# Kernel tuning notes

Measured on AMD Instinct MI355X. Metric: run time of the kernel, lower is better.

Reference implementation:

```python
import jax, jax.numpy as jnp
import numpy as np

NEG_SLOPE = 0.2  # PyG GATConv default negative_slope
N_NODES = 10000
N_EDGES = 320000
IN_CH = 512
HID = 128
HEADS = 4
N_CLASSES = 2


def gat_conv(x, src, dst, n, W, att_src, att_dst, bias, concat):
    """PyG-style GATConv (shared weights for src/dst, eval mode: no dropout)."""
    H, C = att_src.shape
    h = (x @ W).reshape(-1, H, C)                      # [N, H, C]
    a_src = jnp.sum(h * att_src[None], axis=-1)        # [N, H]
    a_dst = jnp.sum(h * att_dst[None], axis=-1)        # [N, H]
    e = a_src[src] + a_dst[dst]                        # [E, H]
    e = jnp.where(e > 0, e, NEG_SLOPE * e)             # LeakyReLU
    # numerically stable softmax over incoming edges of each dst node
    m = jax.ops.segment_max(e, dst, num_segments=n)    # [N, H]
    m = jnp.where(jnp.isfinite(m), m, 0.0)
    ex = jnp.exp(e - m[dst])
    denom = jax.ops.segment_sum(ex, dst, num_segments=n)
    alpha = ex / (denom[dst] + 1e-16)                  # [E, H]
    out = jax.ops.segment_sum(alpha[:, :, None] * h[src], dst, num_segments=n)  # [N,H,C]
    if concat:
        out = out.reshape(n, H * C)
    else:
        out = out.mean(axis=1)
    return out + bias


def setup_inputs() -> dict:
    key = jax.random.key(0)
    ks = jax.random.split(key, 8)
    x = jax.random.normal(ks[0], (N_NODES, IN_CH), dtype=jnp.float32)
    edge_index = jax.random.randint(ks[1], (2, N_EDGES), 0, N_NODES, dtype=jnp.int32)
    s1 = 1.0 / np.sqrt(IN_CH)
    s2 = 1.0 / np.sqrt(HEADS * HID)
    return {
        "x": x,
        "edge_index": edge_index,
        "W1": jax.random.normal(ks[2], (IN_CH, HEADS * HID), dtype=jnp.float32) * s1,
        "att_src1": jax.random.normal(ks[3], (HEADS, HID), dtype=jnp.float32) * s2,
        "att_dst1": jax.random.normal(ks[4], (HEADS, HID), dtype=jnp.float32) * s2,
        "b1": jnp.zeros((HEADS * HID,), dtype=jnp.float32),
        "W2": jax.random.normal(ks[5], (HEADS * HID, N_CLASSES), dtype=jnp.float32) * s2,
        "att_src2": jax.random.normal(ks[6], (1, N_CLASSES), dtype=jnp.float32),
        "att_dst2": jax.random.normal(ks[7], (1, N_CLASSES), dtype=jnp.float32),
        "b2": jnp.zeros((N_CLASSES,), dtype=jnp.float32),
    }


def reference(x, edge_index, W1, att_src1, att_dst1, b1, W2, att_src2, att_dst2, b2):
    n = x.shape[0]
    loop = jnp.arange(n, dtype=edge_index.dtype)       # PyG add_self_loops=True
    src = jnp.concatenate([edge_index[0], loop])
    dst = jnp.concatenate([edge_index[1], loop])
    h = gat_conv(x, src, dst, n, W1, att_src1, att_dst1, b1, concat=True)
    h = jax.nn.elu(h)
    out = gat_conv(h, src, dst, n, W2, att_src2, att_dst2, b2, concat=False)
    return out
```

## Files before the change

kernel.cpp:

```cpp
#include <hip/hip_runtime.h>
#include <hip/hip_bf16.h>

#define N_NODES 10000
#define N_EDGES 320000
#define E_TOT   330000
#define IN_CH   512
#define F1      512
#define HID     128
#define HEADS   4
#define SLOTS   128
#define MAXDEG  64

typedef __attribute__((ext_vector_type(8))) short bf16x8;
typedef __attribute__((ext_vector_type(4))) float f32x4;

__device__ __forceinline__ float lo16(unsigned u) { return __uint_as_float(u << 16); }
__device__ __forceinline__ float hi16(unsigned u) { return __uint_as_float(u & 0xffff0000u); }
__device__ __forceinline__ unsigned short bfbits(float f) {
    __hip_bfloat16 h = __float2bfloat16(f);
    return *(unsigned short*)&h;
}

__device__ __forceinline__ void gload_lds16(const void* g, void* l) {
    __builtin_amdgcn_global_load_lds(
        (const __attribute__((address_space(1))) unsigned int*)g,
        (__attribute__((address_space(3))) unsigned int*)l, 16, 0, 0);
}

__global__ void k_prep(const float* __restrict__ x, unsigned short* __restrict__ xb,
                       const float* __restrict__ w1, unsigned short* __restrict__ w1t,
                       int* __restrict__ zbase) {
    __shared__ float tile[64][65];
    int b = blockIdx.x;
    int t = threadIdx.x;
    if (b < 5000) {
        int idx = b * 256 + t;
        float4 v = ((const float4*)x)[idx];
        ushort4 u;
        u.x = bfbits(v.x); u.y = bfbits(v.y); u.z = bfbits(v.z); u.w = bfbits(v.w);
        ((ushort4*)xb)[idx] = u;
    } else if (b < 5064) {
        int bb = b - 5000;
        int bi = bb >> 3, bj = bb & 7;
        int r0 = t >> 6, col = t & 63;
#pragma unroll
        for (int p = 0; p < 16; ++p) {
            int row = p * 4 + r0;
            tile[row][col] = w1[(size_t)(bi * 64 + row) * 512 + bj * 64 + col];
        }
        __syncthreads();
#pragma unroll
        for (int p = 0; p < 16; ++p) {
            int row = p * 4 + r0;
            w1t[(size_t)(bj * 64 + row) * 512 + bi * 64 + col] = bfbits(tile[col][row]);
        }
    } else {
        int idx = (b - 5064) * 256 + t;
        if (idx < 130000) zbase[idx] = 0;
    }
}

#define GEMM_BLKS 316
__device__ __forceinline__ void gemm_step(const __hip_bfloat16* A, const __hip_bfloat16* B,
                                          int wr, int wc, int col16, int quad,
                                          f32x4 acc[4][4]) {
#pragma unroll
    for (int kk = 0; kk < 2; ++kk) {
        bf16x8 af[4], bf[4];
#pragma unroll
        for (int m = 0; m < 4; ++m) {
            int r = wr * 64 + m * 16 + col16;
            af[m] = *(const bf16x8*)((const char*)A + r * 128 +
                                     ((kk * 64 + quad * 16) ^ ((r & 7) << 4)));
        }
#pragma unroll
        for (int c = 0; c < 4; ++c) {
            int r = wc * 64 + c * 16 + col16;
            bf[c] = *(const bf16x8*)((const char*)B + r * 128 +
                                     ((kk * 64 + quad * 16) ^ ((r & 7) << 4)));
        }
#pragma unroll
        for (int m = 0; m < 4; ++m)
#pragma unroll
            for (int c = 0; c < 4; ++c)
                acc[m][c] = __builtin_amdgcn_mfma_f32_16x16x32_bf16(af[m], bf[c], acc[m][c], 0, 0, 0);
    }
}

__global__ __launch_bounds__(256) void k_gemm1(const __hip_bfloat16* __restrict__ xb,
                                               const __hip_bfloat16* __restrict__ w1t,
                                               const float* __restrict__ as_vec,
                                               const float* __restrict__ ad_vec,
                                               __hip_bfloat16* __restrict__ h1b,
                                               float* __restrict__ a_src,
                                               float* __restrict__ a_dst,
                                               const int* __restrict__ src,
                                               const int* __restrict__ dst,
                                               int* __restrict__ cnt,
                                               int* __restrict__ slots) {
    if (blockIdx.x >= GEMM_BLKS) {
        int e = (blockIdx.x - GEMM_BLKS) * 256 + threadIdx.x;
        if (e < E_TOT) {
            int d, s;
            if (e < N_EDGES) { d = dst[e]; s = src[e]; } else { d = e - N_EDGES; s = d; }
            int pos = atomicAdd(&cnt[d], 1);
            if (pos < SLOTS) slots[d * SLOTS + pos] = s;
        }
        return;
    }
    __shared__ __align__(16) __hip_bfloat16 lsA[2][128 * 64];
    __shared__ __align__(16) __hip_bfloat16 lsB[2][128 * 64];
    int nt = blockIdx.x & 3;
    int mt = blockIdx.x >> 2;
    int row0 = mt * 128;
    int t = threadIdx.x;
    int lane = t & 63;
    int wid = t >> 6;
    int wr = wid >> 1, wc = wid & 1;
    int col16 = lane & 15, quad = lane >> 4;

    const __hip_bfloat16* ga[4];
    const __hip_bfloat16* gb[4];
    unsigned loff[4];
#pragma unroll
    for (int p = 0; p < 4; ++p) {
        int ci = p * 256 + t;
        int row = ci >> 3, ch = ci & 7;
        int sch = ch ^ (row & 7);
        ga[p] = xb + (size_t)min(row0 + row, N_NODES - 1) * IN_CH + sch * 8;
        gb[p] = w1t + (size_t)(nt * 128 + row) * IN_CH + sch * 8;
        loff[p] = ci * 16;
    }

    f32x4 acc[4][4] = {};

#pragma unroll
    for (int p = 0; p < 4; ++p) gload_lds16(ga[p], (char*)lsA[0] + loff[p]);
#pragma unroll
    for (int p = 0; p < 4; ++p) gload_lds16(gb[p], (char*)lsB[0] + loff[p]);
    __syncthreads();

#pragma unroll 1
    for (int s = 0; s < 7; ++s) {
        int nb = (s + 1) & 1, kt = (s + 1) * 64;
#pragma unroll
        for (int p = 0; p < 4; ++p) gload_lds16(ga[p] + kt, (char*)lsA[nb] + loff[p]);
#pragma unroll
        for (int p = 0; p < 4; ++p) gload_lds16(gb[p] + kt, (char*)lsB[nb] + loff[p]);
        gemm_step(lsA[s & 1], lsB[s & 1], wr, wc, col16, quad, acc);
        __syncthreads();
    }
    gemm_step(lsA[1], lsB[1], wr, wc, col16, quad, acc);

    float asv[4], adv[4];
#pragma unroll
    for (int c = 0; c < 4; ++c) {
        int col = nt * 128 + wc * 64 + c * 16 + col16;
        asv[c] = as_vec[col];
        adv[c] = ad_vec[col];
    }
#pragma unroll
    for (int m = 0; m < 4; ++m) {
#pragma unroll
        for (int reg = 0; reg < 4; ++reg) {
            int row = row0 + wr * 64 + m * 16 + quad * 4 + reg;
            bool ok = row < N_NODES;
            float ps = 0.f, pd = 0.f;
#pragma unroll
            for (int c = 0; c < 4; ++c) {
                float v = acc[m][c][reg];
                ps += v * asv[c];
                pd += v * adv[c];
                if (ok) h1b[(size_t)row * F1 + nt * 128 + wc * 64 + c * 16 + col16] =
                            __float2bfloat16(v);
            }
#pragma unroll
            for (int off = 1; off <= 8; off <<= 1) {
                ps += __shfl_xor(ps, off);
                pd += __shfl_xor(pd, off);
            }
            if (col16 == 0 && ok) {
                atomicAdd(&a_src[row * HEADS + nt], ps);
                atomicAdd(&a_dst[row * HEADS + nt], pd);
            }
        }
    }
}

__global__ __launch_bounds__(256, 8) void k_aggr1(const __hip_bfloat16* __restrict__ h1b,
                                               const float* __restrict__ a_src,
                                               const float* __restrict__ a_dst,
                                               const int* __restrict__ cnt,
                                               const int* __restrict__ slots,
                                               const float* __restrict__ b1,
                                               const float* __restrict__ w2,
                                               const float* __restrict__ as2,
                                               const float* __restrict__ ad2,
                                               float* __restrict__ h2,
                                               float* __restrict__ a_src2,
                                               float* __restrict__ a_dst2) {
    __shared__ int2 wlds[4][MAXDEG];
    int h = blockIdx.x & 3;
    int wslot = threadIdx.x >> 6;
    int n = (blockIdx.x >> 2) * 4 + wslot;
    int lane = threadIdx.x & 63;
    int cn = min(cnt[n], MAXDEG);
    const int* sl = slots + n * SLOTS;
    float adst = a_dst[n * HEADS + h];

    int jc = min(lane, cn - 1);
    int s = sl[jc];
    float e = a_src[s * HEADS + h] + adst;
    e = fmaxf(e, 0.2f * e);
    float w = (lane < cn) ? __expf(e) : 0.f;
    float dsum = w;
#pragma unroll
    for (int off = 1; off < 64; off <<= 1) dsum += __shfl_xor(dsum, off);
    int2 pw; pw.x = s << 10;
    pw.y = __float_as_int(w);
    wlds[wslot][lane] = pw;
    __syncthreads();

    int q = lane >> 4, c16 = lane & 15;
    const char* hb = (const char*)h1b + (h * 128 + c16 * 8) * 2;
    float acc[8] = {};
#pragma unroll 1
    for (int base = 0; base < cn; base += 16) {
        int2 p[4];
#pragma unroll
        for (int k = 0; k < 4; ++k) p[k] = wlds[wslot][base + k * 4 + q];
        uint4 d[4];
#pragma unroll
        for (int k = 0; k < 4; ++k) d[k] = *(const uint4*)(hb + p[k].x);
#pragma unroll
        for (int k = 0; k < 4; ++k) {
            float ww = __int_as_float(p[k].y);
            acc[0] += ww * lo16(d[k].x); acc[1] += ww * hi16(d[k].x);
            acc[2] += ww * lo16(d[k].y); acc[3] += ww * hi16(d[k].y);
            acc[4] += ww * lo16(d[k].z); acc[5] += ww * hi16(d[k].z);
            acc[6] += ww * lo16(d[k].w); acc[7] += ww * hi16(d[k].w);
        }
    }
#pragma unroll
    for (int j = 0; j < 8; ++j) {
        acc[j] += __shfl_xor(acc[j], 16);
        acc[j] += __shfl_xor(acc[j], 32);
    }
    float inv = 1.f / (dsum + 1e-16f);
    int c0 = h * 128 + c16 * 8;
    float ps0 = 0.f, ps1 = 0.f;
#pragma unroll
    for (int j = 0; j < 8; ++j) {
        float v = acc[j] * inv + b1[c0 + j];
        v = v > 0.f ? v : __expf(v) - 1.f;
        ps0 += v * w2[(c0 + j) * 2 + 0];
        ps1 += v * w2[(c0 + j) * 2 + 1];
    }
#pragma unroll
    for (int off = 1; off <= 8; off <<= 1) {
        ps0 += __shfl_xor(ps0, off);
        ps1 += __shfl_xor(ps1, off);
    }
    if (lane == 0) {
        atomicAdd(&h2[n * 2 + 0], ps0);
        atomicAdd(&h2[n * 2 + 1], ps1);
        atomicAdd(&a_src2[n], ps0 * as2[0] + ps1 * as2[1]);
        atomicAdd(&a_dst2[n], ps0 * ad2[0] + ps1 * ad2[1]);
    }
}

__global__ __launch_bounds__(256) void k_aggr2(const float* __restrict__ h2,
                                               const float* __restrict__ a_src2,
                                               const float* __restrict__ a_dst2,
                                               const int* __restrict__ cnt,
                                               const int* __restrict__ slots,
                                               const float* __restrict__ b2,
                                               float* __restrict__ out) {
    int lane = threadIdx.x & 63;
    int sub = lane >> 4, slot = lane & 15;
    int n = blockIdx.x * 16 + (threadIdx.x >> 6) * 4 + sub;
    int cn = min(cnt[n], SLOTS);
    const int* sl = slots + n * SLOTS;
    float adst = a_dst2[n];
    float dsum = 0.f, acc0 = 0.f, acc1 = 0.f;
    for (int i = slot; i < cn; i += 16) {
        int s = sl[i];
        float e = a_src2[s] + adst;
        e = fmaxf(e, 0.2f * e);
        float w = __expf(e);
        dsum += w;
        acc0 += w * h2[s * 2 + 0];
        acc1 += w * h2[s * 2 + 1];
    }
#pragma unroll
    for (int off = 1; off <= 8; off <<= 1) {
        dsum += __shfl_xor(dsum, off);
        acc0 += __shfl_xor(acc0, off);
        acc1 += __shfl_xor(acc1, off);
    }
    if (slot == 0) {
        float inv = 1.f / (dsum + 1e-16f);
        out[n * 2 + 0] = acc0 * inv + b2[0];
        out[n * 2 + 1] = acc1 * inv + b2[1];
    }
}

extern "C" void kernel_launch(void* const* d_in, const int* in_sizes, int n_in,
                              void* d_out, int out_size, void* d_ws, size_t ws_size,
                              hipStream_t stream) {
    const float* x   = (const float*)d_in[0];
    const int*   ei  = (const int*)d_in[1];
    const float* W1  = (const float*)d_in[2];
    const float* as1 = (const float*)d_in[3];
    const float* ad1 = (const float*)d_in[4];
    const float* b1  = (const float*)d_in[5];
    const float* W2  = (const float*)d_in[6];
    const float* as2 = (const float*)d_in[7];
    const float* ad2 = (const float*)d_in[8];
    const float* b2  = (const float*)d_in[9];

    char* ws = (char*)d_ws;
    __hip_bfloat16* h1b = (__hip_bfloat16*)(ws);
    __hip_bfloat16* xb  = (__hip_bfloat16*)(ws + 10240000);
    __hip_bfloat16* w1t = (__hip_bfloat16*)(ws + 20480000);
    const size_t S = 21004288;
    float* a_src1 = (float*)(ws + S);
    float* a_dst1 = (float*)(ws + S + 160000);
    float* h2     = (float*)(ws + S + 320000);
    float* a_src2 = (float*)(ws + S + 400000);
    float* a_dst2 = (float*)(ws + S + 440000);
    int*   cnt    = (int*)(ws + S + 480000);
    int*   slots  = (int*)(ws + S + 520000);

    const int* srcArr = ei;
    const int* dstArr = ei + N_EDGES;

    k_prep<<<5064 + 508, 256, 0, stream>>>(x, (unsigned short*)xb, W1,
                                           (unsigned short*)w1t, (int*)a_src1);
    k_gemm1<<<GEMM_BLKS + 1290, 256, 0, stream>>>(xb, w1t, as1, ad1, h1b,
                                                  a_src1, a_dst1,
                                                  srcArr, dstArr, cnt, slots);
    k_aggr1<<<N_NODES, 256, 0, stream>>>(h1b, a_src1, a_dst1, cnt, slots, b1,
                                         W2, as2, ad2, h2, a_src2, a_dst2);
    k_aggr2<<<N_NODES / 16, 256, 0, stream>>>(h2, a_src2, a_dst2, cnt, slots, b2,
                                              (float*)d_out);
}
```

Before: 167.7 us.

## Process all four heads per wavefront in layer-1 aggregation, drop atomics

k_aggr1 now assigns one wavefront per node covering all four heads: each lane gathers a full 16-byte slice of the 1024-byte h1 row per edge, while the per-head softmax weights are computed once with float4 loads and stored in LDS. Because one wave now owns the whole node, the layer-2 projections are written directly instead of via atomicAdd. That in turn lets the prep kernel zero a smaller region, since h2, a_src2 and a_dst2 are moved past it. The gather loop now walks 4 edges per iteration instead of 16 per 4 lanes, which may reduce memory-level parallelism, and the occupancy hint is lowered from 8 to 4.

```diff
diff --git a/kernel.cpp b/kernel.cpp
--- a/kernel.cpp
+++ b/kernel.cpp
@@ -56,7 +56,7 @@
         }
     } else {
         int idx = (b - 5064) * 256 + t;
-        if (idx < 130000) zbase[idx] = 0;
+        if (idx < 90000) zbase[idx] = 0;
     }
 }
 
@@ -187,7 +187,7 @@
     }
 }
 
-__global__ __launch_bounds__(256, 8) void k_aggr1(const __hip_bfloat16* __restrict__ h1b,
+__global__ __launch_bounds__(256, 4) void k_aggr1(const __hip_bfloat16* __restrict__ h1b,
                                                const float* __restrict__ a_src,
                                                const float* __restrict__ a_dst,
                                                const int* __restrict__ cnt,
@@ -199,55 +199,68 @@
                                                float* __restrict__ h2,
                                                float* __restrict__ a_src2,
                                                float* __restrict__ a_dst2) {
-    __shared__ int2 wlds[4][MAXDEG];
-    int h = blockIdx.x & 3;
-    int wslot = threadIdx.x >> 6;
-    int n = (blockIdx.x >> 2) * 4 + wslot;
+    __shared__ float wlds[4][MAXDEG][4];
+    __shared__ int   olds[4][MAXDEG];
+    int w = threadIdx.x >> 6;
+    int n = blockIdx.x * 4 + w;
     int lane = threadIdx.x & 63;
     int cn = min(cnt[n], MAXDEG);
     const int* sl = slots + n * SLOTS;
-    float adst = a_dst[n * HEADS + h];
 
     int jc = min(lane, cn - 1);
     int s = sl[jc];
-    float e = a_src[s * HEADS + h] + adst;
-    e = fmaxf(e, 0.2f * e);
-    float w = (lane < cn) ? __expf(e) : 0.f;
-    float dsum = w;
-#pragma unroll
-    for (int off = 1; off < 64; off <<= 1) dsum += __shfl_xor(dsum, off);
-    int2 pw; pw.x = s << 10;
-    pw.y = __float_as_int(w);
-    wlds[wslot][lane] = pw;
+    float4 av = *(const float4*)(a_src + s * 4);
+    float4 dv = *(const float4*)(a_dst + n * 4);
+    float e0 = av.x + dv.x; e0 = fmaxf(e0, 0.2f * e0);
+    float e1 = av.y + dv.y; e1 = fmaxf(e1, 0.2f * e1);
+    float e2 = av.z + dv.z; e2 = fmaxf(e2, 0.2f * e2);
+    float e3 = av.w + dv.w; e3 = fmaxf(e3, 0.2f * e3);
+    bool live = lane < cn;
+    float w0 = live ? __expf(e0) : 0.f;
+    float w1 = live ? __expf(e1) : 0.f;
+    float w2w = live ? __expf(e2) : 0.f;
+    float w3 = live ? __expf(e3) : 0.f;
+    float d0 = w0, d1 = w1, d2 = w2w, d3 = w3;
+#pragma unroll
+    for (int off = 1; off < 64; off <<= 1) {
+        d0 += __shfl_xor(d0, off);
+        d1 += __shfl_xor(d1, off);
+        d2 += __shfl_xor(d2, off);
+        d3 += __shfl_xor(d3, off);
+    }
+    olds[w][lane] = s << 10;
+    wlds[w][lane][0] = w0;
+    wlds[w][lane][1] = w1;
+    wlds[w][lane][2] = w2w;
+    wlds[w][lane][3] = w3;
     __syncthreads();
 
-    int q = lane >> 4, c16 = lane & 15;
-    const char* hb = (const char*)h1b + (h * 128 + c16 * 8) * 2;
+    int myh = lane >> 4;
+    const char* hb = (const char*)h1b + lane * 16;
     float acc[8] = {};
 #pragma unroll 1
-    for (int base = 0; base < cn; base += 16) {
-        int2 p[4];
-#pragma unroll
-        for (int k = 0; k < 4; ++k) p[k] = wlds[wslot][base + k * 4 + q];
+    for (int base = 0; base < cn; base += 4) {
+        int off[4];
+        float wk[4];
         uint4 d[4];
 #pragma unroll
-        for (int k = 0; k < 4; ++k) d[k] = *(const uint4*)(hb + p[k].x);
+        for (int k = 0; k < 4; ++k) off[k] = olds[w][base + k];
+#pragma unroll
+        for (int k = 0; k < 4; ++k) wk[k] = wlds[w][base + k][myh];
+#pragma unroll
+        for (int k = 0; k < 4; ++k) d[k] = *(const uint4*)(hb + off[k]);
 #pragma unroll
         for (int k = 0; k < 4; ++k) {
-            float ww = __int_as_float(p[k].y);
+            float ww = wk[k];
             acc[0] += ww * lo16(d[k].x); acc[1] += ww * hi16(d[k].x);
             acc[2] += ww * lo16(d[k].y); acc[3] += ww * hi16(d[k].y);
             acc[4] += ww * lo16(d[k].z); acc[5] += ww * hi16(d[k].z);
             acc[6] += ww * lo16(d[k].w); acc[7] += ww * hi16(d[k].w);
         }
     }
-#pragma unroll
-    for (int j = 0; j < 8; ++j) {
-        acc[j] += __shfl_xor(acc[j], 16);
-        acc[j] += __shfl_xor(acc[j], 32);
-    }
-    float inv = 1.f / (dsum + 1e-16f);
-    int c0 = h * 128 + c16 * 8;
+    float dh = myh == 0 ? d0 : (myh == 1 ? d1 : (myh == 2 ? d2 : d3));
+    float inv = 1.f / (dh + 1e-16f);
+    int c0 = lane * 8;
     float ps0 = 0.f, ps1 = 0.f;
 #pragma unroll
     for (int j = 0; j < 8; ++j) {
@@ -257,15 +270,15 @@
         ps1 += v * w2[(c0 + j) * 2 + 1];
     }
 #pragma unroll
-    for (int off = 1; off <= 8; off <<= 1) {
+    for (int off = 1; off < 64; off <<= 1) {
         ps0 += __shfl_xor(ps0, off);
         ps1 += __shfl_xor(ps1, off);
     }
     if (lane == 0) {
-        atomicAdd(&h2[n * 2 + 0], ps0);
-        atomicAdd(&h2[n * 2 + 1], ps1);
-        atomicAdd(&a_src2[n], ps0 * as2[0] + ps1 * as2[1]);
-        atomicAdd(&a_dst2[n], ps0 * ad2[0] + ps1 * ad2[1]);
+        h2[n * 2 + 0] = ps0;
+        h2[n * 2 + 1] = ps1;
+        a_src2[n] = ps0 * as2[0] + ps1 * as2[1];
+        a_dst2[n] = ps0 * ad2[0] + ps1 * ad2[1];
     }
 }
 
@@ -326,22 +339,22 @@
     const size_t S = 21004288;
     float* a_src1 = (float*)(ws + S);
     float* a_dst1 = (float*)(ws + S + 160000);
-    float* h2     = (float*)(ws + S + 320000);
-    float* a_src2 = (float*)(ws + S + 400000);
-    float* a_dst2 = (float*)(ws + S + 440000);
-    int*   cnt    = (int*)(ws + S + 480000);
+    int*   cnt    = (int*)(ws + S + 320000);
+    float* h2     = (float*)(ws + S + 360000);
+    float* a_src2 = (float*)(ws + S + 440000);
+    float* a_dst2 = (float*)(ws + S + 480000);
     int*   slots  = (int*)(ws + S + 520000);
 
     const int* srcArr = ei;
     const int* dstArr = ei + N_EDGES;
 
-    k_prep<<<5064 + 508, 256, 0, stream>>>(x, (unsigned short*)xb, W1,
+    k_prep<<<5064 + 352, 256, 0, stream>>>(x, (unsigned short*)xb, W1,
                                            (unsigned short*)w1t, (int*)a_src1);
     k_gemm1<<<GEMM_BLKS + 1290, 256, 0, stream>>>(xb, w1t, as1, ad1, h1b,
                                                   a_src1, a_dst1,
                                                   srcArr, dstArr, cnt, slots);
-    k_aggr1<<<N_NODES, 256, 0, stream>>>(h1b, a_src1, a_dst1, cnt, slots, b1,
-                                         W2, as2, ad2, h2, a_src2, a_dst2);
+    k_aggr1<<<N_NODES / 4, 256, 0, stream>>>(h1b, a_src1, a_dst1, cnt, slots, b1,
+                                             W2, as2, ad2, h2, a_src2, a_dst2);
     k_aggr2<<<N_NODES / 16, 256, 0, stream>>>(h2, a_src2, a_dst2, cnt, slots, b2,
                                               (float*)d_out);
 }
```

Result: faster. 161.2 us (-3.9%).

## Software-pipeline gather loads in GAT aggregation and store attention scores head-major

Applied to the files above, without the earlier changes.

Restructures the layer-1 aggregation loop so each wave keeps two sets of neighbour-row gathers in flight (A/B double buffering), loading the next rows before consuming the current ones. This is meant to hide gather latency. It also drops the block-wide barrier, since each wave only reads its own LDS row. The per-node attention scores a_src/a_dst move to a head-major layout so the per-head score lookups are contiguous. Launch bounds are relaxed from 8 to 4 waves per SIMD, trading occupancy for the extra registers the prefetched data needs.

```diff
diff --git a/kernel.cpp b/kernel.cpp
--- a/kernel.cpp
+++ b/kernel.cpp
@@ -180,14 +180,23 @@
                 pd += __shfl_xor(pd, off);
             }
             if (col16 == 0 && ok) {
-                atomicAdd(&a_src[row * HEADS + nt], ps);
-                atomicAdd(&a_dst[row * HEADS + nt], pd);
+                atomicAdd(&a_src[nt * N_NODES + row], ps);
+                atomicAdd(&a_dst[nt * N_NODES + row], pd);
             }
         }
     }
 }
 
-__global__ __launch_bounds__(256, 8) void k_aggr1(const __hip_bfloat16* __restrict__ h1b,
+#define CONSUME(D, W)                                                   \
+    do {                                                                \
+        float ww_ = (W);                                                \
+        acc[0] += ww_ * lo16((D).x); acc[1] += ww_ * hi16((D).x);       \
+        acc[2] += ww_ * lo16((D).y); acc[3] += ww_ * hi16((D).y);       \
+        acc[4] += ww_ * lo16((D).z); acc[5] += ww_ * hi16((D).z);       \
+        acc[6] += ww_ * lo16((D).w); acc[7] += ww_ * hi16((D).w);       \
+    } while (0)
+
+__global__ __launch_bounds__(256, 4) void k_aggr1(const __hip_bfloat16* __restrict__ h1b,
                                                const float* __restrict__ a_src,
                                                const float* __restrict__ a_dst,
                                                const int* __restrict__ cnt,
@@ -201,44 +210,57 @@
                                                float* __restrict__ a_dst2) {
     __shared__ int2 wlds[4][MAXDEG];
     int h = blockIdx.x & 3;
-    int wslot = threadIdx.x >> 6;
-    int n = (blockIdx.x >> 2) * 4 + wslot;
+    int w = threadIdx.x >> 6;
+    int n = (blockIdx.x >> 2) * 4 + w;
     int lane = threadIdx.x & 63;
+    const int* sl = slots + n * SLOTS;
+
+    int s_raw = sl[lane];
     int cn = min(cnt[n], MAXDEG);
-    const int* sl = slots + n * SLOTS;
-    float adst = a_dst[n * HEADS + h];
-
-    int jc = min(lane, cn - 1);
-    int s = sl[jc];
-    float e = a_src[s * HEADS + h] + adst;
+    float adst = a_dst[h * N_NODES + n];
+    bool live = lane < cn;
+    int s = live ? s_raw : 0;
+    float e = a_src[h * N_NODES + s] + adst;
     e = fmaxf(e, 0.2f * e);
-    float w = (lane < cn) ? __expf(e) : 0.f;
-    float dsum = w;
+    float wgt = live ? __expf(e) : 0.f;
+    float dsum = wgt;
 #pragma unroll
     for (int off = 1; off < 64; off <<= 1) dsum += __shfl_xor(dsum, off);
     int2 pw; pw.x = s << 10;
-    pw.y = __float_as_int(w);
-    wlds[wslot][lane] = pw;
-    __syncthreads();
+    pw.y = __float_as_int(wgt);
+    wlds[w][lane] = pw;
 
     int q = lane >> 4, c16 = lane & 15;
-    const char* hb = (const char*)h1b + (h * 128 + c16 * 8) * 2;
+    const char* hb = (const char*)h1b + h * 256 + c16 * 16;
     float acc[8] = {};
+    int kmax = (cn + 3) >> 2;
+    int np = (kmax + 1) >> 1;
+    int i1 = min(1, np - 1);
+    int2 pA0 = wlds[w][q],            pA1 = wlds[w][4 + q];
+    uint4 dA0 = *(const uint4*)(hb + pA0.x);
+    uint4 dA1 = *(const uint4*)(hb + pA1.x);
+    int2 pB0 = wlds[w][i1 * 8 + q],   pB1 = wlds[w][i1 * 8 + 4 + q];
+    uint4 dB0 = *(const uint4*)(hb + pB0.x);
+    uint4 dB1 = *(const uint4*)(hb + pB1.x);
 #pragma unroll 1
-    for (int base = 0; base < cn; base += 16) {
-        int2 p[4];
-#pragma unroll
-        for (int k = 0; k < 4; ++k) p[k] = wlds[wslot][base + k * 4 + q];
-        uint4 d[4];
-#pragma unroll
-        for (int k = 0; k < 4; ++k) d[k] = *(const uint4*)(hb + p[k].x);
-#pragma unroll
-        for (int k = 0; k < 4; ++k) {
-            float ww = __int_as_float(p[k].y);
-            acc[0] += ww * lo16(d[k].x); acc[1] += ww * hi16(d[k].x);
-            acc[2] += ww * lo16(d[k].y); acc[3] += ww * hi16(d[k].y);
-            acc[4] += ww * lo16(d[k].z); acc[5] += ww * hi16(d[k].z);
-            acc[6] += ww * lo16(d[k].w); acc[7] += ww * hi16(d[k].w);
+    for (int i = 0; i < np; i += 2) {
+        CONSUME(dA0, __int_as_float(pA0.y));
+        CONSUME(dA1, __int_as_float(pA1.y));
+        int nxa = i + 2;
+        if (nxa < np) {
+            pA0 = wlds[w][nxa * 8 + q]; pA1 = wlds[w][nxa * 8 + 4 + q];
+            dA0 = *(const uint4*)(hb + pA0.x);
+            dA1 = *(const uint4*)(hb + pA1.x);
+        }
+        if (i + 1 < np) {
+            CONSUME(dB0, __int_as_float(pB0.y));
+            CONSUME(dB1, __int_as_float(pB1.y));
+            int nxb = i + 3;
+            if (nxb < np) {
+                pB0 = wlds[w][nxb * 8 + q]; pB1 = wlds[w][nxb * 8 + 4 + q];
+                dB0 = *(const uint4*)(hb + pB0.x);
+                dB1 = *(const uint4*)(hb + pB1.x);
+            }
         }
     }
 #pragma unroll
```

Result: faster. 157.5 us (-6.1%).
